# Kernel tuning notes

Hardware: AMD Instinct MI355X
Metric: run time of the kernel (lower is better)

Reference implementation:

```python
import jax, jax.numpy as jnp
import numpy as np

DIM = 512
HEADS = 8
HEAD_DIM = 64
MAX_FREQ = 256.0


def axial_freqs(H, W, head_dim, max_freq=MAX_FREQ):
    # rotary-embedding-torch: per-axis rotary dim = head_dim // 2, freqs_for='pixel'
    r = head_dim // 2
    base = jnp.linspace(1.0, max_freq / 2.0, r // 2) * jnp.pi  # (r/2,)
    ph = jnp.linspace(-1.0, 1.0, H)
    pw = jnp.linspace(-1.0, 1.0, W)
    fh = jnp.repeat(ph[:, None] * base[None, :], 2, axis=-1)  # (H, r) interleaved repeat
    fw = jnp.repeat(pw[:, None] * base[None, :], 2, axis=-1)  # (W, r)
    fh = jnp.broadcast_to(fh[:, None, :], (H, W, r))
    fw = jnp.broadcast_to(fw[None, :, :], (H, W, r))
    return jnp.concatenate([fh, fw], axis=-1)  # (H, W, head_dim)


def rotate_half(t):
    # interleaved pairs: (x1, x2) -> (-x2, x1)
    shp = t.shape
    t = t.reshape(*shp[:-1], -1, 2)
    return jnp.stack((-t[..., 1], t[..., 0]), axis=-1).reshape(shp)


def apply_rope(t, freqs):
    # freqs: (H, W, d) broadcast over (BT, h, H, W, d)
    return t * jnp.cos(freqs) + rotate_half(t) * jnp.sin(freqs)


def setup_inputs() -> dict:
    key = jax.random.key(0)
    k1, k2, k3 = jax.random.split(key, 3)
    B, T, H, W, D = 2, 8, 32, 32, DIM
    inner = HEADS * HEAD_DIM
    x = jax.random.normal(k1, (B, T, H, W, D), dtype=jnp.float32)
    w_qkv = jax.random.normal(k2, (3 * inner, D), dtype=jnp.float32) * (D ** -0.5)
    w_out = jax.random.normal(k3, (D, inner), dtype=jnp.float32) * (inner ** -0.5)
    b_out = jnp.zeros((D,), dtype=jnp.float32)
    return {"x": x, "w_qkv": w_qkv, "w_out": w_out, "b_out": b_out}


def reference(x, w_qkv, w_out, b_out):
    B, T, H, W, D = x.shape
    h, d = HEADS, HEAD_DIM
    qkv = jnp.einsum('bthwc,fc->bthwf', x, w_qkv)  # (B,T,H,W,3*inner)
    q, k, v = jnp.split(qkv, 3, axis=-1)

    def to_heads(t):
        # B T H W (h d) -> (B T) h H W d
        t = t.reshape(B * T, H, W, h, d)
        return jnp.transpose(t, (0, 3, 1, 2, 4))

    q, k, v = to_heads(q), to_heads(k), to_heads(v)
    freqs = axial_freqs(H, W, d)
    q = apply_rope(q, freqs)
    k = apply_rope(k, freqs)

    q = q.reshape(B * T, h, H * W, d)
    k = k.reshape(B * T, h, H * W, d)
    v = v.reshape(B * T, h, H * W, d)

    scale = d ** -0.5
    logits = jnp.einsum('bhnd,bhmd->bhnm', q, k) * scale
    attn = jax.nn.softmax(logits, axis=-1)
    out = jnp.einsum('bhnm,bhmd->bhnd', attn, v)  # (BT, h, HW, d)

    # (B T) h (H W) d -> B T H W (h d)
    out = out.reshape(B, T, h, H, W, d)
    out = jnp.transpose(out, (0, 1, 3, 4, 2, 5)).reshape(B, T, H, W, h * d)
    return jnp.einsum('bthwf,df->bthwd', out, w_out) + b_out
```

## Files before the change

kernel.cpp:

```cpp
#include <hip/hip_runtime.h>
#include <math.h>

#define NH 8
#define HD 64
#define NSEQ 1024
#define DMODEL 512
#define F3 1536
#define NTOK 16384
#define BH 128
#define KVP 72
#define TP 136
#define QSCALE 0.1803368867f

typedef __attribute__((ext_vector_type(8))) short bf16x8;
typedef __attribute__((ext_vector_type(4))) float f32x4;
typedef __attribute__((ext_vector_type(16))) float f32x16;
typedef __attribute__((ext_vector_type(4))) unsigned int u32x4;
#define MFMA16(a, b, c) __builtin_amdgcn_mfma_f32_16x16x32_bf16(a, b, c, 0, 0, 0)
#define MFMA32(a, b, c) __builtin_amdgcn_mfma_f32_32x32x16_bf16(a, b, c, 0, 0, 0)

__device__ __forceinline__ float freq_of(int j) {
    return 3.14159265358979323846f * (1.0f + (float)j * (127.0f / 15.0f));
}
__device__ __forceinline__ unsigned short bf16_rtn(float x) {
    unsigned u = __builtin_bit_cast(unsigned, x);
    return (unsigned short)((u + 0x7FFF + ((u >> 16) & 1)) >> 16);
}
__device__ __forceinline__ int swz(int r) { return (r & 3) ^ ((r >> 2) & 3); }

__global__ __launch_bounds__(256) void cvt2_kernel(
        const float* __restrict__ wq, unsigned short* __restrict__ wq_bf,
        const float* __restrict__ wo, unsigned short* __restrict__ wo_bf) {
    const int b = blockIdx.x;
    const float* src;
    unsigned short* dst;
    int i;
    if (b < F3 * DMODEL / 1024) { src = wq; dst = wq_bf; i = b * 256 + threadIdx.x; }
    else { src = wo; dst = wo_bf; i = (b - F3 * DMODEL / 1024) * 256 + threadIdx.x; }
    const float4 v = ((const float4*)src)[i];
    ((ushort4*)dst)[i] = make_ushort4(bf16_rtn(v.x), bf16_rtn(v.y),
                                      bf16_rtn(v.z), bf16_rtn(v.w));
}

template<int PLANES, int NREP>
__device__ __forceinline__ void gemm_reg_pipe(
        const unsigned short* __restrict__ a_hi, const unsigned short* __restrict__ a_lo,
        const unsigned short* __restrict__ b_bf,
        char* lds, int m0, int f0, int t, f32x4 (&acc)[NREP][4][4]) {
    const int w = t >> 6, lane = t & 63, l15 = lane & 15, quad = lane >> 4;
    const int mw = (w & 1) * 64, nw = (w >> 1) * 64;
    const int APL = PLANES - 1;
    const int NPL = APL + NREP;
    const int STAGE = NPL * 4096;
    const int r = t >> 1;
    const int g0 = (t & 1) * 2;

    uint4 regs[NPL][2];
    auto load_regs = [&](int kt) {
        const int k0 = kt * 32;
        #pragma unroll
        for (int p = 0; p < NPL; p++) {
            const unsigned short* src = (p < APL) ? (p == 0 ? a_hi : a_lo) : b_bf;
            const int row0 = (p < APL) ? m0 : (f0 + (p - APL) * 128);
            const unsigned short* g = src + (size_t)(row0 + r) * DMODEL + k0 + g0 * 8;
            regs[p][0] = *(const uint4*)g;
            regs[p][1] = *(const uint4*)(g + 8);
        }
    };
    auto store_lds = [&](int stage) {
        unsigned short* S = (unsigned short*)lds + stage * STAGE;
        const int s0 = ((g0 ^ swz(r))) * 8;
        const int s1 = (((g0 + 1) ^ swz(r))) * 8;
        #pragma unroll
        for (int p = 0; p < NPL; p++) {
            unsigned short* Sp = S + p * 4096 + r * 32;
            *(uint4*)&Sp[s0] = regs[p][0];
            *(uint4*)&Sp[s1] = regs[p][1];
        }
    };

    load_regs(0);
    store_lds(0);
    for (int kt = 0; kt < 16; kt++) {
        __syncthreads();
        if (kt < 15) load_regs(kt + 1);
        const unsigned short* S = (const unsigned short*)lds + (kt & 1) * STAGE;
        bf16x8 ah[4], al[4];
        #pragma unroll
        for (int mt = 0; mt < 4; mt++) {
            const int rr = mw + mt * 16 + l15;
            const int off = rr * 32 + (quad ^ swz(rr)) * 8;
            ah[mt] = *(const bf16x8*)&S[off];
            if (APL == 2) al[mt] = *(const bf16x8*)&S[4096 + off];
        }
        #pragma unroll
        for (int nr = 0; nr < NREP; nr++) {
            bf16x8 bb[4];
            #pragma unroll
            for (int nt = 0; nt < 4; nt++) {
                const int rr = nw + nt * 16 + l15;
                bb[nt] = *(const bf16x8*)&S[(APL + nr) * 4096 + rr * 32
                                            + (quad ^ swz(rr)) * 8];
            }
            #pragma unroll
            for (int mt = 0; mt < 4; mt++)
                #pragma unroll
                for (int nt = 0; nt < 4; nt++) {
                    acc[nr][mt][nt] = MFMA16(ah[mt], bb[nt], acc[nr][mt][nt]);
                    if (APL == 2) acc[nr][mt][nt] = MFMA16(al[mt], bb[nt], acc[nr][mt][nt]);
                }
        }
        if (kt < 15) store_lds((kt + 1) & 1);
    }
    __syncthreads();
}

__device__ __forceinline__ void gemm_pipe_qkv(
        const float* __restrict__ x, const unsigned short* __restrict__ b_bf,
        char* lds, int m0, int f0, int t, f32x4 (&acc)[2][4][4]) {
    const int w = t >> 6, lane = t & 63, l15 = lane & 15, quad = lane >> 4;
    const int mw = (w & 1) * 64, nw = (w >> 1) * 64;
    const int STAGE = 3 * 4096;
    const int r = t >> 1;
    const int g0 = (t & 1) * 2;

    float4 af[4];
    uint4 bregs[2][2];
    auto load_regs = [&](int kt) {
        const int k0 = kt * 32;
        const float* gA = x + (size_t)(m0 + r) * DMODEL + k0 + g0 * 8;
        #pragma unroll
        for (int i = 0; i < 4; i++) af[i] = ((const float4*)gA)[i];
        #pragma unroll
        for (int p = 0; p < 2; p++) {
            const unsigned short* g =
                b_bf + (size_t)(f0 + p * 128 + r) * DMODEL + k0 + g0 * 8;
            bregs[p][0] = *(const uint4*)g;
            bregs[p][1] = *(const uint4*)(g + 8);
        }
    };
    auto store_lds = [&](int stage) {
        unsigned short* S = (unsigned short*)lds + stage * STAGE;
        const int s0 = ((g0 ^ swz(r))) * 8;
        const int s1 = (((g0 + 1) ^ swz(r))) * 8;
        auto cvt8 = [](const float4 a, const float4 b) {
            const float f[8] = {a.x, a.y, a.z, a.w, b.x, b.y, b.z, b.w};
            unsigned hw[4];
            #pragma unroll
            for (int j = 0; j < 4; j++)
                hw[j] = (unsigned)bf16_rtn(f[2 * j])
                      | ((unsigned)bf16_rtn(f[2 * j + 1]) << 16);
            return make_uint4(hw[0], hw[1], hw[2], hw[3]);
        };
        unsigned short* Sa = S + r * 32;
        *(uint4*)&Sa[s0] = cvt8(af[0], af[1]);
        *(uint4*)&Sa[s1] = cvt8(af[2], af[3]);
        #pragma unroll
        for (int p = 0; p < 2; p++) {
            unsigned short* Sp = S + (1 + p) * 4096 + r * 32;
            *(uint4*)&Sp[s0] = bregs[p][0];
            *(uint4*)&Sp[s1] = bregs[p][1];
        }
    };

    load_regs(0);
    store_lds(0);
    for (int kt = 0; kt < 16; kt++) {
        __syncthreads();
        if (kt < 15) load_regs(kt + 1);
        const unsigned short* S = (const unsigned short*)lds + (kt & 1) * STAGE;
        bf16x8 ah[4];
        #pragma unroll
        for (int mt = 0; mt < 4; mt++) {
            const int rr = mw + mt * 16 + l15;
            ah[mt] = *(const bf16x8*)&S[rr * 32 + (quad ^ swz(rr)) * 8];
        }
        #pragma unroll
        for (int nr = 0; nr < 2; nr++) {
            bf16x8 bb[4];
            #pragma unroll
            for (int nt = 0; nt < 4; nt++) {
                const int rr = nw + nt * 16 + l15;
                bb[nt] = *(const bf16x8*)&S[(1 + nr) * 4096 + rr * 32
                                            + (quad ^ swz(rr)) * 8];
            }
            #pragma unroll
            for (int mt = 0; mt < 4; mt++)
                #pragma unroll
                for (int nt = 0; nt < 4; nt++)
                    acc[nr][mt][nt] = MFMA16(ah[mt], bb[nt], acc[nr][mt][nt]);
        }
        if (kt < 15) store_lds((kt + 1) & 1);
    }
    __syncthreads();
}

__global__ __launch_bounds__(256, 3) void qkv_mfma_kernel(
        const float* __restrict__ x, const unsigned short* __restrict__ wq_bf,
        unsigned short* __restrict__ q_bf, unsigned short* __restrict__ k_bf,
        unsigned short* __restrict__ v_th) {
    __shared__ __align__(16) char lds[49152 + 4608];
    unsigned short* T = (unsigned short*)lds;
    float* t_cy = (float*)(lds + 49152);
    float* t_sy = t_cy + 64;
    float* t_cx = t_sy + 64;
    float* t_sx = t_cx + 512;

    const int m0 = blockIdx.x * 128;
    const int f0 = blockIdx.y * 256;
    const int t = threadIdx.x;
    const int w = t >> 6, lane = t & 63, l15 = lane & 15, quad = lane >> 4;
    const int mw = (w & 1) * 64, nw = (w >> 1) * 64;
    const int sel = f0 >> 9;
    const int bt = m0 >> 10;
    const int n0 = m0 & 1023;

    if (sel != 2) {
        for (int idx = t; idx < 576; idx += 256) {
            if (idx < 64) {
                const int yi = idx >> 4, j = idx & 15;
                const float pos = -1.0f + (float)((n0 >> 5) + yi) * (2.0f / 31.0f);
                float sv, cv; sincosf(pos * freq_of(j), &sv, &cv);
                t_sy[idx] = sv; t_cy[idx] = cv;
            } else {
                const int k2 = idx - 64, xi = k2 >> 4, j = k2 & 15;
                const float pos = -1.0f + (float)xi * (2.0f / 31.0f);
                float sv, cv; sincosf(pos * freq_of(j), &sv, &cv);
                t_sx[k2] = sv; t_cx[k2] = cv;
            }
        }
    }
    __syncthreads();

    f32x4 acc[2][4][4];
    #pragma unroll
    for (int nr = 0; nr < 2; nr++)
        #pragma unroll
        for (int mt = 0; mt < 4; mt++)
            #pragma unroll
            for (int nt = 0; nt < 4; nt++) acc[nr][mt][nt] = (f32x4){0.f, 0.f, 0.f, 0.f};

    gemm_pipe_qkv(x, wq_bf, lds, m0, f0, t, acc);

    #pragma unroll
    for (int nr = 0; nr < 2; nr++) {
        const int fs = f0 + nr * 128;
        if (sel != 2) {
            const float post = (sel == 0) ? QSCALE : 1.0f;
            #pragma unroll
            for (int mt = 0; mt < 4; mt++)
                #pragma unroll
                for (int nt = 0; nt < 4; nt++)
                    #pragma unroll
                    for (int rr = 0; rr < 4; rr++) {
                        const int ml = mw + mt * 16 + quad * 4 + rr;
                        const int dd = (nw + nt * 16 + l15) & 63;
                        const int j0 = (dd & 31) >> 1;
                        float c, s;
                        if (dd < 32) { c = t_cy[(ml >> 5) * 16 + j0]; s = t_sy[(ml >> 5) * 16 + j0]; }
                        else         { c = t_cx[(ml & 31) * 16 + j0]; s = t_sx[(ml & 31) * 16 + j0]; }
                        const float v = acc[nr][mt][nt][rr];
                        const float pv = __shfl_xor(v, 1);
                        acc[nr][mt][nt][rr] =
                            ((l15 & 1) ? (v * c + pv * s) : (v * c - pv * s)) * post;
                    }
        }

        if (sel == 2) {
            #pragma unroll
            for (int mt = 0; mt < 4; mt++)
                #pragma unroll
                for (int nt = 0; nt < 4; nt++) {
                    const int fl = nw + nt * 16 + l15;
                    const int mlb = mw + mt * 16 + quad * 4;
                    ushort4 pk = make_ushort4(
                        bf16_rtn(acc[nr][mt][nt][0]), bf16_rtn(acc[nr][mt][nt][1]),
                        bf16_rtn(acc[nr][mt][nt][2]), bf16_rtn(acc[nr][mt][nt][3]));
                    *(ushort4*)&T[fl * TP + mlb] = pk;
                }
        } else {
            #pragma unroll
            for (int mt = 0; mt < 4; mt++)
                #pragma unroll
                for (int nt = 0; nt < 4; nt++)
                    #pragma unroll
                    for (int rr = 0; rr < 4; rr++) {
                        const int ml = mw + mt * 16 + quad * 4 + rr;
                        const int fl = nw + nt * 16 + l15;
                        T[ml * TP + fl] = bf16_rtn(acc[nr][mt][nt][rr]);
                    }
        }
        __syncthreads();
        if (sel == 2) {
            #pragma unroll
            for (int p = 0; p < 8; p++) {
                const int idx = p * 256 + t;
                const int fl = idx >> 4, g8 = (idx & 15) * 8;
                const int head = ((fs + fl) >> 6) & 7;
                *(uint4*)(v_th + ((size_t)(bt * NH + head) * HD + ((fs + fl) & 63)) * NSEQ
                          + n0 + g8) = *(const uint4*)&T[fl * TP + g8];
            }
        } else {
            unsigned short* dst = (sel == 0) ? q_bf : k_bf;
            #pragma unroll
            for (int p = 0; p < 8; p++) {
                const int idx = p * 256 + t;
                const int ml = idx >> 4, g8 = (idx & 15) * 8;
                const int head = ((fs + g8) >> 6) & 7;
                *(uint4*)(dst + ((size_t)(bt * NH + head) * NSEQ + n0 + ml) * HD
                          + ((fs + g8) & 63)) = *(const uint4*)&T[ml * TP + g8];
            }
        }
        __syncthreads();
    }
}

__global__ __launch_bounds__(256, 2) void attn_kernel(
        const unsigned short* __restrict__ q_bf, const unsigned short* __restrict__ k_bf,
        const unsigned short* __restrict__ v_th,
        unsigned short* __restrict__ o_bf) {
    __shared__ unsigned short Ks[2][64 * KVP];
    __shared__ unsigned short Vs[2][64 * KVP];

    const int bh = blockIdx.x;
    const int qt = blockIdx.y;
    const int t = threadIdx.x;
    const int w = t >> 6;
    const int lane = t & 63;
    const int l31 = lane & 31;
    const int hi = lane >> 5;

    const size_t bh_nd = (size_t)bh * NSEQ * HD;
    const size_t bh_dn = (size_t)bh * HD * NSEQ;

    bf16x8 qfB[2][4];
    #pragma unroll
    for (int mf = 0; mf < 2; mf++) {
        const size_t rbase =
            bh_nd + (size_t)(qt * 256 + w * 64 + mf * 32 + l31) * HD + hi * 8;
        #pragma unroll
        for (int ds = 0; ds < 4; ds++)
            qfB[mf][ds] = *(const bf16x8*)(q_bf + rbase + ds * 16);
    }

    uint4 kr[2], vr[2];
    auto load_kv = [&](int kt) {
        #pragma unroll
        for (int p = 0; p < 2; p++) {
            const int cc = t + p * 256;
            const int r = cc >> 3, off8 = (cc & 7) * 8;
            kr[p] = *(const uint4*)(k_bf + bh_nd + (size_t)(kt * 64 + r) * HD + off8);
            vr[p] = *(const uint4*)(v_th + bh_dn + (size_t)r * NSEQ + kt * 64 + off8);
        }
    };
    auto store_kv = [&](int st) {
        #pragma unroll
        for (int p = 0; p < 2; p++) {
            const int cc = t + p * 256;
            const int r = cc >> 3, off8 = (cc & 7) * 8;
            *(uint4*)&Ks[st][r * KVP + off8] = kr[p];
            *(uint4*)&Vs[st][r * KVP + off8] = vr[p];
        }
    };

    const bf16x8 ones = {(short)0x3F80, (short)0x3F80, (short)0x3F80, (short)0x3F80,
                         (short)0x3F80, (short)0x3F80, (short)0x3F80, (short)0x3F80};

    f32x16 o_acc[2][2], l_acc[2];
    #pragma unroll
    for (int i = 0; i < 16; i++) {
        o_acc[0][0][i] = 0.f; o_acc[0][1][i] = 0.f;
        o_acc[1][0][i] = 0.f; o_acc[1][1][i] = 0.f;
        l_acc[0][i] = 0.f; l_acc[1][i] = 0.f;
    }

    load_kv(0);
    store_kv(0);
    for (int kt = 0; kt < 16; kt++) {
        __syncthreads();
        if (kt < 15) load_kv(kt + 1);
        const unsigned short* K = Ks[kt & 1];
        const unsigned short* V = Vs[kt & 1];

        #pragma unroll
        for (int nt2 = 0; nt2 < 2; nt2++) {
            bf16x8 kb[4];
            #pragma unroll
            for (int ds = 0; ds < 4; ds++)
                kb[ds] = *(const bf16x8*)&K[(nt2 * 32 + l31) * KVP + ds * 16 + hi * 8];

            u32x4 paw[2][2];
            #pragma unroll
            for (int mf = 0; mf < 2; mf++) {
                f32x16 s;
                #pragma unroll
                for (int i = 0; i < 16; i++) s[i] = 0.f;
                #pragma unroll
                for (int ds = 0; ds < 4; ds++) s = MFMA32(kb[ds], qfB[mf][ds], s);

                unsigned wv[8];
                #pragma unroll
                for (int i = 0; i < 8; i++) {
                    const float p0 = exp2f(s[2 * i]);
                    const float p1 = exp2f(s[2 * i + 1]);
                    asm("v_cvt_pk_bf16_f32 %0, %1, %2" : "=v"(wv[i]) : "v"(p0), "v"(p1));
                }
                asm volatile("v_permlane32_swap_b32 %0, %1" : "+v"(wv[0]), "+v"(wv[2]));
                asm volatile("v_permlane32_swap_b32 %0, %1" : "+v"(wv[1]), "+v"(wv[3]));
                asm volatile("v_permlane32_swap_b32 %0, %1" : "+v"(wv[4]), "+v"(wv[6]));
                asm volatile("v_permlane32_swap_b32 %0, %1" : "+v"(wv[5]), "+v"(wv[7]));
                paw[mf][0] = (u32x4){wv[0], wv[1], wv[2], wv[3]};
                paw[mf][1] = (u32x4){wv[4], wv[5], wv[6], wv[7]};
            }

            #pragma unroll
            for (int k2 = 0; k2 < 2; k2++) {
                bf16x8 vb[2];
                #pragma unroll
                for (int dt = 0; dt < 2; dt++)
                    vb[dt] = *(const bf16x8*)&V[(dt * 32 + l31) * KVP
                                 + (nt2 * 2 + k2) * 16 + hi * 8];
                #pragma unroll
                for (int mf = 0; mf < 2; mf++) {
                    const bf16x8 pa = __builtin_bit_cast(bf16x8, paw[mf][k2]);
                    l_acc[mf] = MFMA32(pa, ones, l_acc[mf]);
                    #pragma unroll
                    for (int dt = 0; dt < 2; dt++)
                        o_acc[mf][dt] = MFMA32(pa, vb[dt], o_acc[mf][dt]);
                }
            }
        }
        if (kt < 15) store_kv((kt + 1) & 1);
    }

    __syncthreads();
    unsigned short* Osh = &Ks[0][0];
    #pragma unroll
    for (int mf = 0; mf < 2; mf++)
        #pragma unroll
        for (int r = 0; r < 16; r++) {
            const float inv = 1.0f / l_acc[mf][r];
            const int row = w * 64 + mf * 32 + (r & 3) + 8 * (r >> 2) + 4 * hi;
            #pragma unroll
            for (int dt = 0; dt < 2; dt++)
                Osh[row * KVP + dt * 32 + l31] = bf16_rtn(o_acc[mf][dt][r] * inv);
        }
    __syncthreads();
    const int btq = bh >> 3, head = bh & 7;
    #pragma unroll
    for (int p = 0; p < 8; p++) {
        const int idx = p * 256 + t;
        const int row = idx >> 3, g8 = (idx & 7) * 8;
        *(uint4*)(o_bf + ((size_t)(btq * NSEQ + qt * 256 + row)) * DMODEL
                  + head * HD + g8) = *(const uint4*)&Osh[row * KVP + g8];
    }
}

__global__ __launch_bounds__(256, 2) void proj_mfma_kernel(
        const unsigned short* __restrict__ o_bf,
        const unsigned short* __restrict__ wo_bf,
        const float* __restrict__ b_out, float* __restrict__ out) {
    __shared__ __align__(16) char lds[49152];

    const int m0 = blockIdx.x * 128;
    const int f0 = blockIdx.y * 256;
    const int t = threadIdx.x;
    const int w = t >> 6, lane = t & 63, l15 = lane & 15, quad = lane >> 4;
    const int mw = (w & 1) * 64, nw = (w >> 1) * 64;

    f32x4 acc[2][4][4];
    #pragma unroll
    for (int nr = 0; nr < 2; nr++)
        #pragma unroll
        for (int mt = 0; mt < 4; mt++)
            #pragma unroll
            for (int nt = 0; nt < 4; nt++) acc[nr][mt][nt] = (f32x4){0.f, 0.f, 0.f, 0.f};

    gemm_reg_pipe<2, 2>(o_bf, o_bf, wo_bf, lds, m0, f0, t, acc);

    #pragma unroll
    for (int nr = 0; nr < 2; nr++) {
        const int fs = f0 + nr * 128;
        float bias_v[4];
        #pragma unroll
        for (int nt = 0; nt < 4; nt++) bias_v[nt] = b_out[fs + nw + nt * 16 + l15];
        #pragma unroll
        for (int mt = 0; mt < 4; mt++)
            #pragma unroll
            for (int nt = 0; nt < 4; nt++)
                #pragma unroll
                for (int rr = 0; rr < 4; rr++) {
                    const int m = m0 + mw + mt * 16 + quad * 4 + rr;
                    out[(size_t)m * DMODEL + fs + nw + nt * 16 + l15] =
                        acc[nr][mt][nt][rr] + bias_v[nt];
                }
    }
}

extern "C" void kernel_launch(void* const* d_in, const int* in_sizes, int n_in,
                              void* d_out, int out_size, void* d_ws, size_t ws_size,
                              hipStream_t stream) {
    const float* x  = (const float*)d_in[0];
    const float* wq = (const float*)d_in[1];
    const float* wo = (const float*)d_in[2];
    const float* bo = (const float*)d_in[3];
    float* out = (float*)d_out;

    const size_t per = (size_t)BH * NSEQ * HD;
    unsigned short* o_bf = (unsigned short*)d_ws;
    unsigned short* q_bf = o_bf + per;
    unsigned short* k_bf = q_bf + per;
    unsigned short* v_th = k_bf + per;
    unsigned short* wq_bf = v_th + per;
    unsigned short* wo_bf = wq_bf + (size_t)F3 * DMODEL;

    cvt2_kernel<<<dim3((F3 * DMODEL + DMODEL * DMODEL) / 1024), 256, 0, stream>>>(
        wq, wq_bf, wo, wo_bf);
    qkv_mfma_kernel<<<dim3(NTOK / 128, F3 / 256), 256, 0, stream>>>(
        x, wq_bf, q_bf, k_bf, v_th);
    attn_kernel<<<dim3(BH, 4), 256, 0, stream>>>(
        q_bf, k_bf, v_th, o_bf);
    proj_mfma_kernel<<<dim3(NTOK / 128, DMODEL / 256), 256, 0, stream>>>(
        o_bf, wo_bf, bo, out);
}
```

Measured before the change: 218.3 us.

## Split attention block into 8 waves of 32 query rows, sum softmax denominator in VALU

Result: faster. 206.8 us (median of 2 runs) (-5.3%).

```diff
diff --git a/kernel.cpp b/kernel.cpp
--- a/kernel.cpp
+++ b/kernel.cpp
@@ -315,12 +315,13 @@
     }
 }
 
-__global__ __launch_bounds__(256, 2) void attn_kernel(
+__global__ __launch_bounds__(512, 2) void attn_kernel(
         const unsigned short* __restrict__ q_bf, const unsigned short* __restrict__ k_bf,
         const unsigned short* __restrict__ v_th,
         unsigned short* __restrict__ o_bf) {
     __shared__ unsigned short Ks[2][64 * KVP];
     __shared__ unsigned short Vs[2][64 * KVP];
+    __shared__ float Lsh[256];
 
     const int bh = blockIdx.x;
     const int qt = blockIdx.y;
@@ -333,45 +334,31 @@
     const size_t bh_nd = (size_t)bh * NSEQ * HD;
     const size_t bh_dn = (size_t)bh * HD * NSEQ;
 
-    bf16x8 qfB[2][4];
-    #pragma unroll
-    for (int mf = 0; mf < 2; mf++) {
+    bf16x8 qfB[4];
+    {
         const size_t rbase =
-            bh_nd + (size_t)(qt * 256 + w * 64 + mf * 32 + l31) * HD + hi * 8;
+            bh_nd + (size_t)(qt * 256 + w * 32 + l31) * HD + hi * 8;
         #pragma unroll
         for (int ds = 0; ds < 4; ds++)
-            qfB[mf][ds] = *(const bf16x8*)(q_bf + rbase + ds * 16);
-    }
-
-    uint4 kr[2], vr[2];
+            qfB[ds] = *(const bf16x8*)(q_bf + rbase + ds * 16);
+    }
+
+    const int sr = t >> 3, soff = (t & 7) * 8;
+    uint4 kr, vr;
     auto load_kv = [&](int kt) {
-        #pragma unroll
-        for (int p = 0; p < 2; p++) {
-            const int cc = t + p * 256;
-            const int r = cc >> 3, off8 = (cc & 7) * 8;
-            kr[p] = *(const uint4*)(k_bf + bh_nd + (size_t)(kt * 64 + r) * HD + off8);
-            vr[p] = *(const uint4*)(v_th + bh_dn + (size_t)r * NSEQ + kt * 64 + off8);
-        }
+        kr = *(const uint4*)(k_bf + bh_nd + (size_t)(kt * 64 + sr) * HD + soff);
+        vr = *(const uint4*)(v_th + bh_dn + (size_t)sr * NSEQ + kt * 64 + soff);
     };
     auto store_kv = [&](int st) {
-        #pragma unroll
-        for (int p = 0; p < 2; p++) {
-            const int cc = t + p * 256;
-            const int r = cc >> 3, off8 = (cc & 7) * 8;
-            *(uint4*)&Ks[st][r * KVP + off8] = kr[p];
-            *(uint4*)&Vs[st][r * KVP + off8] = vr[p];
-        }
+        *(uint4*)&Ks[st][sr * KVP + soff] = kr;
+        *(uint4*)&Vs[st][sr * KVP + soff] = vr;
     };
 
-    const bf16x8 ones = {(short)0x3F80, (short)0x3F80, (short)0x3F80, (short)0x3F80,
-                         (short)0x3F80, (short)0x3F80, (short)0x3F80, (short)0x3F80};
-
-    f32x16 o_acc[2][2], l_acc[2];
+    f32x16 o_acc[2], zero16;
+    float l_sum = 0.f;
     #pragma unroll
     for (int i = 0; i < 16; i++) {
-        o_acc[0][0][i] = 0.f; o_acc[0][1][i] = 0.f;
-        o_acc[1][0][i] = 0.f; o_acc[1][1][i] = 0.f;
-        l_acc[0][i] = 0.f; l_acc[1][i] = 0.f;
+        o_acc[0][i] = 0.f; o_acc[1][i] = 0.f; zero16[i] = 0.f;
     }
 
     load_kv(0);
@@ -389,67 +376,67 @@
             for (int ds = 0; ds < 4; ds++)
                 kb[ds] = *(const bf16x8*)&K[(nt2 * 32 + l31) * KVP + ds * 16 + hi * 8];
 
-            u32x4 paw[2][2];
-            #pragma unroll
-            for (int mf = 0; mf < 2; mf++) {
-                f32x16 s;
-                #pragma unroll
-                for (int i = 0; i < 16; i++) s[i] = 0.f;
-                #pragma unroll
-                for (int ds = 0; ds < 4; ds++) s = MFMA32(kb[ds], qfB[mf][ds], s);
-
-                unsigned wv[8];
-                #pragma unroll
-                for (int i = 0; i < 8; i++) {
-                    const float p0 = exp2f(s[2 * i]);
-                    const float p1 = exp2f(s[2 * i + 1]);
-                    asm("v_cvt_pk_bf16_f32 %0, %1, %2" : "=v"(wv[i]) : "v"(p0), "v"(p1));
+            __builtin_amdgcn_s_setprio(1);
+            f32x16 s = MFMA32(kb[0], qfB[0], zero16);
+            #pragma unroll
+            for (int ds = 1; ds < 4; ds++) s = MFMA32(kb[ds], qfB[ds], s);
+            __builtin_amdgcn_s_setprio(0);
+
+            unsigned wv[8];
+            float pp[8];
+            #pragma unroll
+            for (int i = 0; i < 8; i++) {
+                const float p0 = exp2f(s[2 * i]);
+                const float p1 = exp2f(s[2 * i + 1]);
+                pp[i] = p0 + p1;
+                asm("v_cvt_pk_bf16_f32 %0, %1, %2" : "=v"(wv[i]) : "v"(p0), "v"(p1));
+            }
+            l_sum += ((pp[0] + pp[1]) + (pp[2] + pp[3]))
+                   + ((pp[4] + pp[5]) + (pp[6] + pp[7]));
+
+            asm volatile("v_permlane32_swap_b32 %0, %1" : "+v"(wv[0]), "+v"(wv[2]));
+            asm volatile("v_permlane32_swap_b32 %0, %1" : "+v"(wv[1]), "+v"(wv[3]));
+            asm volatile("v_permlane32_swap_b32 %0, %1" : "+v"(wv[4]), "+v"(wv[6]));
+            asm volatile("v_permlane32_swap_b32 %0, %1" : "+v"(wv[5]), "+v"(wv[7]));
+
+            __builtin_amdgcn_s_setprio(1);
+            #pragma unroll
+            for (int k2 = 0; k2 < 2; k2++) {
+                const u32x4 paw = {wv[k2 * 4 + 0], wv[k2 * 4 + 1],
+                                   wv[k2 * 4 + 2], wv[k2 * 4 + 3]};
+                const bf16x8 pa = __builtin_bit_cast(bf16x8, paw);
+                #pragma unroll
+                for (int dt = 0; dt < 2; dt++) {
+                    const bf16x8 vb = *(const bf16x8*)&V[(dt * 32 + l31) * KVP
+                                         + (nt2 * 2 + k2) * 16 + hi * 8];
+                    o_acc[dt] = MFMA32(pa, vb, o_acc[dt]);
                 }
-                asm volatile("v_permlane32_swap_b32 %0, %1" : "+v"(wv[0]), "+v"(wv[2]));
-                asm volatile("v_permlane32_swap_b32 %0, %1" : "+v"(wv[1]), "+v"(wv[3]));
-                asm volatile("v_permlane32_swap_b32 %0, %1" : "+v"(wv[4]), "+v"(wv[6]));
-                asm volatile("v_permlane32_swap_b32 %0, %1" : "+v"(wv[5]), "+v"(wv[7]));
-                paw[mf][0] = (u32x4){wv[0], wv[1], wv[2], wv[3]};
-                paw[mf][1] = (u32x4){wv[4], wv[5], wv[6], wv[7]};
-            }
-
-            #pragma unroll
-            for (int k2 = 0; k2 < 2; k2++) {
-                bf16x8 vb[2];
-                #pragma unroll
-                for (int dt = 0; dt < 2; dt++)
-                    vb[dt] = *(const bf16x8*)&V[(dt * 32 + l31) * KVP
-                                 + (nt2 * 2 + k2) * 16 + hi * 8];
-                #pragma unroll
-                for (int mf = 0; mf < 2; mf++) {
-                    const bf16x8 pa = __builtin_bit_cast(bf16x8, paw[mf][k2]);
-                    l_acc[mf] = MFMA32(pa, ones, l_acc[mf]);
-                    #pragma unroll
-                    for (int dt = 0; dt < 2; dt++)
-                        o_acc[mf][dt] = MFMA32(pa, vb[dt], o_acc[mf][dt]);
-                }
-            }
+            }
+            __builtin_amdgcn_s_setprio(0);
         }
         if (kt < 15) store_kv((kt + 1) & 1);
     }
 
+    l_sum += __shfl_xor(l_sum, 32);
+    const float inv = 1.0f / l_sum;
+    if (hi == 0) Lsh[w * 32 + l31] = inv;
     __syncthreads();
+
     unsigned short* Osh = &Ks[0][0];
     #pragma unroll
-    for (int mf = 0; mf < 2; mf++)
-        #pragma unroll
-        for (int r = 0; r < 16; r++) {
-            const float inv = 1.0f / l_acc[mf][r];
-            const int row = w * 64 + mf * 32 + (r & 3) + 8 * (r >> 2) + 4 * hi;
-            #pragma unroll
-            for (int dt = 0; dt < 2; dt++)
-                Osh[row * KVP + dt * 32 + l31] = bf16_rtn(o_acc[mf][dt][r] * inv);
-        }
+    for (int r = 0; r < 16; r++) {
+        const int row32 = (r & 3) + 8 * (r >> 2) + 4 * hi;
+        const float invr = Lsh[w * 32 + row32];
+        const int row = w * 32 + row32;
+        #pragma unroll
+        for (int dt = 0; dt < 2; dt++)
+            Osh[row * KVP + dt * 32 + l31] = bf16_rtn(o_acc[dt][r] * invr);
+    }
     __syncthreads();
     const int btq = bh >> 3, head = bh & 7;
     #pragma unroll
-    for (int p = 0; p < 8; p++) {
-        const int idx = p * 256 + t;
+    for (int p = 0; p < 4; p++) {
+        const int idx = p * 512 + t;
         const int row = idx >> 3, g8 = (idx & 7) * 8;
         *(uint4*)(o_bf + ((size_t)(btq * NSEQ + qt * 256 + row)) * DMODEL
                   + head * HD + g8) = *(const uint4*)&Osh[row * KVP + g8];
@@ -518,7 +505,7 @@
         wq, wq_bf, wo, wo_bf);
     qkv_mfma_kernel<<<dim3(NTOK / 128, F3 / 256), 256, 0, stream>>>(
         x, wq_bf, q_bf, k_bf, v_th);
-    attn_kernel<<<dim3(BH, 4), 256, 0, stream>>>(
+    attn_kernel<<<dim3(BH, 4), 512, 0, stream>>>(
         q_bf, k_bf, v_th, o_bf);
     proj_mfma_kernel<<<dim3(NTOK / 128, DMODEL / 256), 256, 0, stream>>>(
         o_bf, wo_bf, bo, out);
```
